# Kernel tuning notes

Hardware: AMD Instinct MI355X
Metric: run time of the kernel (lower is better)

The kernel has to match this reference:

```python
import jax, jax.numpy as jnp
import numpy as np

N_NODES = 200000
N_EDGES = 6400000
N_GRAPHS = 512
DIM_IN = 128
HID = 32
BN_EPS = 1e-5


def _gin(x, src, dst, w1, b1, w2, b2):
    # GINConv with eps=0: MLP(x + sum_{j in N(i)} x_j)
    agg = jax.ops.segment_sum(x[src], dst, num_segments=N_NODES)
    h = x + agg
    h = jnp.maximum(h @ w1 + b1, 0.0)
    return h @ w2 + b2


def _bn(x, gamma, beta):
    # BatchNorm1d, training mode: batch stats, biased variance
    m = jnp.mean(x, axis=0)
    v = jnp.var(x, axis=0)
    return gamma * (x - m) * jax.lax.rsqrt(v + BN_EPS) + beta


def setup_inputs() -> dict:
    key = jax.random.key(0)
    ks = jax.random.split(key, 20)
    s = 0.1
    inp = {
        "x": jax.random.normal(ks[0], (N_NODES, DIM_IN), jnp.float32),
        "edge_index": jax.random.randint(ks[1], (2, N_EDGES), 0, N_NODES, jnp.int32),
        "batch": jnp.sort(jax.random.randint(ks[2], (N_NODES,), 0, N_GRAPHS, jnp.int32)),
        "e0_w1": s * jax.random.normal(ks[3], (DIM_IN, HID), jnp.float32),
        "e0_b1": s * jax.random.normal(ks[4], (HID,), jnp.float32),
        "e0_w2": s * jax.random.normal(ks[5], (HID, HID), jnp.float32),
        "e0_b2": s * jax.random.normal(ks[6], (HID,), jnp.float32),
        "enc_w1": s * jax.random.normal(ks[7], (4, HID, HID), jnp.float32),
        "enc_b1": s * jax.random.normal(ks[8], (4, HID), jnp.float32),
        "enc_w2": s * jax.random.normal(ks[9], (4, HID, HID), jnp.float32),
        "enc_b2": s * jax.random.normal(ks[10], (4, HID), jnp.float32),
        "enc_gamma": jnp.ones((5, HID), jnp.float32),
        "enc_beta": jnp.zeros((5, HID), jnp.float32),
        "dec_w1": s * jax.random.normal(ks[11], (5, HID, HID), jnp.float32),
        "dec_b1": s * jax.random.normal(ks[12], (5, HID), jnp.float32),
        "dec_w2": s * jax.random.normal(ks[13], (4, HID, HID), jnp.float32),
        "dec_b2": s * jax.random.normal(ks[14], (4, HID), jnp.float32),
        "dec_w2_last": s * jax.random.normal(ks[15], (HID, DIM_IN), jnp.float32),
        "dec_b2_last": s * jax.random.normal(ks[16], (DIM_IN,), jnp.float32),
        "dec_gamma": jnp.ones((4, HID), jnp.float32),
        "dec_beta": jnp.zeros((4, HID), jnp.float32),
    }
    return inp


def reference(x, edge_index, batch,
              e0_w1, e0_b1, e0_w2, e0_b2,
              enc_w1, enc_b1, enc_w2, enc_b2, enc_gamma, enc_beta,
              dec_w1, dec_b1, dec_w2, dec_b2, dec_w2_last, dec_b2_last,
              dec_gamma, dec_beta):
    src, dst = edge_index[0], edge_index[1]

    # ----- Encoder: 5 GIN layers, ReLU then BN, collect per-layer reps -----
    xs = []
    h = jnp.maximum(_gin(x, src, dst, e0_w1, e0_b1, e0_w2, e0_b2), 0.0)
    h = _bn(h, enc_gamma[0], enc_beta[0])
    xs.append(h)
    for i in range(4):
        h = jnp.maximum(_gin(h, src, dst, enc_w1[i], enc_b1[i], enc_w2[i], enc_b2[i]), 0.0)
        h = _bn(h, enc_gamma[i + 1], enc_beta[i + 1])
        xs.append(h)
    encoded_rep = h

    # ----- Decoder: 5 GIN layers, ReLU; BN on all but last -----
    d = encoded_rep
    for i in range(5):
        w2 = dec_w2[i] if i < 4 else dec_w2_last
        b2 = dec_b2[i] if i < 4 else dec_b2_last
        d = jnp.maximum(_gin(d, src, dst, dec_w1[i], dec_b1[i], w2, b2), 0.0)
        if i < 4:
            d = _bn(d, dec_gamma[i], dec_beta[i])
    decoded_rep = d

    # ----- Global add pool of each encoder layer output, concat -----
    xpool = [jax.ops.segment_sum(xi, batch, num_segments=N_GRAPHS) for xi in xs]
    global_rep = jnp.concatenate(xpool, axis=1)  # [G, 5*32]

    return encoded_rep, decoded_rep, global_rep
```

## Files before the change

kernel.cpp:

```cpp
#include <hip/hip_runtime.h>
#include <hip/hip_bf16.h>
#include <hip/hip_fp16.h>
#include <string.h>

#define N_NODES  200000
#define N_EDGES  6400000
#define N_GRAPHS 512
#define DIM_IN   128
#define HID      32
#define BN_EPS   1e-5f

#define CHUNK    2048
#define NCHUNKS  98

typedef const float* fp;

__device__ __forceinline__ unsigned short f2h(float f) {
    __half h = __float2half(f);
    unsigned short u; __builtin_memcpy(&u, &h, 2); return u;
}
__device__ __forceinline__ float2 h2f2(unsigned int u) {
    __half2 h; __builtin_memcpy(&h, &u, 4);
    return __half22float2(h);
}


__global__ __launch_bounds__(256) void k_hist2(const int* __restrict__ dst,
                                               int* __restrict__ deg) {
    __shared__ int lh[12500];
    const int grp = blockIdx.x & 15;
    const int blk = blockIdx.x >> 4;
    const int lo = grp * 12500;
    for (int j = threadIdx.x; j < 12500; j += 256) lh[j] = 0;
    __syncthreads();
    const int4* d4 = reinterpret_cast<const int4*>(dst) + blk * 100000;
    for (int j = threadIdx.x; j < 100000; j += 256) {
        int4 v = d4[j];
        int a;
        a = v.x - lo; if ((unsigned)a < 12500u) atomicAdd(&lh[a], 1);
        a = v.y - lo; if ((unsigned)a < 12500u) atomicAdd(&lh[a], 1);
        a = v.z - lo; if ((unsigned)a < 12500u) atomicAdd(&lh[a], 1);
        a = v.w - lo; if ((unsigned)a < 12500u) atomicAdd(&lh[a], 1);
    }
    __syncthreads();
    for (int j = threadIdx.x; j < 12500; j += 256) {
        int c = lh[j];
        if (c) atomicAdd(&deg[lo + j], c);
    }
}

__global__ void k_chunksum(const int* __restrict__ deg, int* __restrict__ chunksum) {
    __shared__ int red[256];
    int b = blockIdx.x, t = threadIdx.x;
    int base = b * CHUNK;
    int s = 0;
    for (int k = 0; k < 8; ++k) {
        int i = base + t + k * 256;
        if (i < N_NODES) s += deg[i];
    }
    red[t] = s; __syncthreads();
    for (int off = 128; off > 0; off >>= 1) {
        if (t < off) red[t] += red[t + off];
        __syncthreads();
    }
    if (t == 0) chunksum[b] = red[0];
}

__global__ void k_scanchunks(const int* __restrict__ chunksum, int* __restrict__ chunkoff,
                             int* __restrict__ rowptr) {
    __shared__ int buf[128];
    int t = threadIdx.x;
    int v = (t < NCHUNKS) ? chunksum[t] : 0;
    buf[t] = v; __syncthreads();
    for (int off = 1; off < 128; off <<= 1) {
        int add = (t >= off) ? buf[t - off] : 0;
        __syncthreads();
        buf[t] += add;
        __syncthreads();
    }
    if (t < NCHUNKS) chunkoff[t] = buf[t] - v;
    if (t == 0) rowptr[N_NODES] = N_EDGES;
}

__global__ void k_scanfinal(const int* __restrict__ deg, const int* __restrict__ chunkoff,
                            int* __restrict__ rowptr, int* __restrict__ fillpos) {
    __shared__ int tsum[256];
    int b = blockIdx.x, t = threadIdx.x;
    int base = b * CHUNK + t * 8;
    int v[8]; int s = 0;
    for (int k = 0; k < 8; ++k) {
        int i = base + k;
        v[k] = (i < N_NODES) ? deg[i] : 0;
        s += v[k];
    }
    tsum[t] = s; __syncthreads();
    for (int off = 1; off < 256; off <<= 1) {
        int add = (t >= off) ? tsum[t - off] : 0;
        __syncthreads();
        tsum[t] += add;
        __syncthreads();
    }
    int run = tsum[t] - s + chunkoff[b];
    for (int k = 0; k < 8; ++k) {
        int i = base + k;
        if (i < N_NODES) { rowptr[i] = run; fillpos[i] = run; run += v[k]; }
    }
}

__global__ __launch_bounds__(256) void k_fill2(
    const int* __restrict__ src, const int* __restrict__ dst,
    int* __restrict__ fillpos, int* __restrict__ csr)
{
    const int grp = blockIdx.x & 7;
    const int blk = blockIdx.x >> 3;
    const int lo = grp * 25000, hi = lo + 25000;
    const int4* d4 = reinterpret_cast<const int4*>(dst) + blk * 12500;
    const int4* s4 = reinterpret_cast<const int4*>(src) + blk * 12500;
    for (int j = threadIdx.x; j < 12500; j += 256) {
        int4 d = d4[j];
        int4 s = s4[j];
        if (d.x >= lo && d.x < hi) { int p = atomicAdd(&fillpos[d.x], 1); csr[p] = s.x; }
        if (d.y >= lo && d.y < hi) { int p = atomicAdd(&fillpos[d.y], 1); csr[p] = s.y; }
        if (d.z >= lo && d.z < hi) { int p = atomicAdd(&fillpos[d.z], 1); csr[p] = s.z; }
        if (d.w >= lo && d.w < hi) { int p = atomicAdd(&fillpos[d.w], 1); csr[p] = s.w; }
    }
}

__global__ void k_bounds(const int* __restrict__ batch, int* __restrict__ gstart) {
    int g = blockIdx.x * blockDim.x + threadIdx.x;
    if (g > N_GRAPHS) return;
    if (g == N_GRAPHS) { gstart[g] = N_NODES; return; }
    int lo = 0, hi = N_NODES;
    while (lo < hi) {
        int mid = (lo + hi) >> 1;
        if (batch[mid] < g) lo = mid + 1; else hi = mid;
    }
    gstart[g] = lo;
}


__global__ __launch_bounds__(256) void k_proj128(
    const float* __restrict__ x, fp w1, float* __restrict__ y,
    unsigned short* __restrict__ y16)
{
    __shared__ float w1s[DIM_IN * 32];
    for (int i = threadIdx.x; i < DIM_IN * 32; i += 256) w1s[i] = w1[i];
    __syncthreads();
    const int lane = threadIdx.x & 63;
    const int c = lane & 31;
    const int srcBase = lane & 32;
    int worker   = (blockIdx.x * blockDim.x + threadIdx.x) >> 5;
    int nworkers = (gridDim.x * blockDim.x) >> 5;
    for (int n = worker; n < N_NODES; n += nworkers) {
        const float* xr = x + (size_t)n * DIM_IN;
        float x0 = xr[c], x1 = xr[32 + c], x2 = xr[64 + c], x3 = xr[96 + c];
        float acc = 0.f;
        #pragma unroll
        for (int k = 0; k < 32; ++k) {
            acc = fmaf(__shfl(x0, srcBase | k, 64), w1s[k * 32 + c], acc);
            acc = fmaf(__shfl(x1, srcBase | k, 64), w1s[(32 + k) * 32 + c], acc);
            acc = fmaf(__shfl(x2, srcBase | k, 64), w1s[(64 + k) * 32 + c], acc);
            acc = fmaf(__shfl(x3, srcBase | k, 64), w1s[(96 + k) * 32 + c], acc);
        }
        y[(size_t)n * 32 + c] = acc;
        y16[(size_t)n * 32 + c] = f2h(acc);
    }
}


__global__ __launch_bounds__(256) void k_gather16(
    const float* __restrict__ h, const unsigned short* __restrict__ h16,
    const int* __restrict__ rowptr, const int* __restrict__ csr,
    float* __restrict__ sout)
{
    const int lane = threadIdx.x & 63;
    const int sub = lane & 15;
    const int srcBase = lane & 48;
    const unsigned int* hp = reinterpret_cast<const unsigned int*>(h16);
    const float2* hs = reinterpret_cast<const float2*>(h);
    float2* so = reinterpret_cast<float2*>(sout);
    int worker   = (blockIdx.x * blockDim.x + threadIdx.x) >> 4;
    int nworkers = (gridDim.x * blockDim.x) >> 4;
    for (int n = worker; n < N_NODES; n += nworkers) {
        int e0 = rowptr[n], e1 = rowptr[n + 1];
        float2 self = hs[(size_t)n * 16 + sub];
        float a0 = self.x, a1 = self.y;
        int e = e0;
        while (e < e1) {
            int rem = e1 - e;
            int cnt = rem < 16 ? rem : 16;
            int myidx = (sub < cnt) ? csr[e + sub] : 0;
            int k = 0;
            for (; k + 8 <= cnt; k += 8) {
                int i0 = __shfl(myidx, srcBase | (k + 0), 64);
                int i1 = __shfl(myidx, srcBase | (k + 1), 64);
                int i2 = __shfl(myidx, srcBase | (k + 2), 64);
                int i3 = __shfl(myidx, srcBase | (k + 3), 64);
                int i4 = __shfl(myidx, srcBase | (k + 4), 64);
                int i5 = __shfl(myidx, srcBase | (k + 5), 64);
                int i6 = __shfl(myidx, srcBase | (k + 6), 64);
                int i7 = __shfl(myidx, srcBase | (k + 7), 64);
                unsigned int u0 = hp[(size_t)i0 * 16 + sub];
                unsigned int u1 = hp[(size_t)i1 * 16 + sub];
                unsigned int u2 = hp[(size_t)i2 * 16 + sub];
                unsigned int u3 = hp[(size_t)i3 * 16 + sub];
                unsigned int u4 = hp[(size_t)i4 * 16 + sub];
                unsigned int u5 = hp[(size_t)i5 * 16 + sub];
                unsigned int u6 = hp[(size_t)i6 * 16 + sub];
                unsigned int u7 = hp[(size_t)i7 * 16 + sub];
                float2 f0 = h2f2(u0), f1 = h2f2(u1), f2 = h2f2(u2), f3 = h2f2(u3);
                float2 f4 = h2f2(u4), f5 = h2f2(u5), f6 = h2f2(u6), f7 = h2f2(u7);
                a0 += ((f0.x + f1.x) + (f2.x + f3.x)) + ((f4.x + f5.x) + (f6.x + f7.x));
                a1 += ((f0.y + f1.y) + (f2.y + f3.y)) + ((f4.y + f5.y) + (f6.y + f7.y));
            }
            for (; k < cnt; ++k) {
                int s = __shfl(myidx, srcBase | k, 64);
                float2 f = h2f2(hp[(size_t)s * 16 + sub]);
                a0 += f.x; a1 += f.y;
            }
            e += cnt;
        }
        float2 o; o.x = a0; o.y = a1;
        so[(size_t)n * 16 + sub] = o;
    }
}


__global__ __launch_bounds__(256) void k_mlp32(
    float* __restrict__ s, fp w1, fp b1, fp w2, fp b2, float* __restrict__ stats)
{
    const int lane = threadIdx.x & 63;
    const int c = lane & 31;
    const int srcBase = lane & 32;
    float w1r[32], w2r[32];
    #pragma unroll
    for (int k = 0; k < 32; ++k) {
        w1r[k] = w1[k * 32 + c];
        w2r[k] = w2[k * 32 + c];
    }
    const float b1c = b1[c];
    const float b2c = b2[c];
    int worker   = (blockIdx.x * blockDim.x + threadIdx.x) >> 5;
    int nworkers = (gridDim.x * blockDim.x) >> 5;
    float s1 = 0.f, s2 = 0.f;
    for (int n = worker; n < N_NODES; n += nworkers) {
        float sv = s[(size_t)n * 32 + c];
        float acc1 = b1c;
        #pragma unroll
        for (int k = 0; k < 32; ++k)
            acc1 = fmaf(__shfl(sv, srcBase | k, 64), w1r[k], acc1);
        float h3 = fmaxf(acc1, 0.f);
        float acc2 = b2c;
        #pragma unroll
        for (int k = 0; k < 32; ++k)
            acc2 = fmaf(__shfl(h3, srcBase | k, 64), w2r[k], acc2);
        float a = fmaxf(acc2, 0.f);
        s[(size_t)n * 32 + c] = a;
        s1 += a; s2 += a * a;
    }
    s1 += __shfl_xor(s1, 32, 64);
    s2 += __shfl_xor(s2, 32, 64);
    __shared__ float ls1[4][32], ls2[4][32];
    int w = threadIdx.x >> 6;
    if ((threadIdx.x & 32) == 0) { ls1[w][c] = s1; ls2[w][c] = s2; }
    __syncthreads();
    if (threadIdx.x < 32) {
        float t1 = ls1[0][c] + ls1[1][c] + ls1[2][c] + ls1[3][c];
        float t2 = ls2[0][c] + ls2[1][c] + ls2[2][c] + ls2[3][c];
        atomicAdd(&stats[c], t1);
        atomicAdd(&stats[32 + c], t2);
    }
}

__global__ __launch_bounds__(256) void k_mlp0(
    float* __restrict__ s, fp b1, fp w2, fp b2, float* __restrict__ stats)
{
    const int lane = threadIdx.x & 63;
    const int c = lane & 31;
    const int srcBase = lane & 32;
    float w2r[32];
    #pragma unroll
    for (int k = 0; k < 32; ++k) w2r[k] = w2[k * 32 + c];
    const float b1c = b1[c];
    const float b2c = b2[c];
    int worker   = (blockIdx.x * blockDim.x + threadIdx.x) >> 5;
    int nworkers = (gridDim.x * blockDim.x) >> 5;
    float s1 = 0.f, s2 = 0.f;
    for (int n = worker; n < N_NODES; n += nworkers) {
        float sv = s[(size_t)n * 32 + c];
        float h3 = fmaxf(sv + b1c, 0.f);
        float acc2 = b2c;
        #pragma unroll
        for (int k = 0; k < 32; ++k)
            acc2 = fmaf(__shfl(h3, srcBase | k, 64), w2r[k], acc2);
        float a = fmaxf(acc2, 0.f);
        s[(size_t)n * 32 + c] = a;
        s1 += a; s2 += a * a;
    }
    s1 += __shfl_xor(s1, 32, 64);
    s2 += __shfl_xor(s2, 32, 64);
    __shared__ float ls1[4][32], ls2[4][32];
    int w = threadIdx.x >> 6;
    if ((threadIdx.x & 32) == 0) { ls1[w][c] = s1; ls2[w][c] = s2; }
    __syncthreads();
    if (threadIdx.x < 32) {
        float t1 = ls1[0][c] + ls1[1][c] + ls1[2][c] + ls1[3][c];
        float t2 = ls2[0][c] + ls2[1][c] + ls2[2][c] + ls2[3][c];
        atomicAdd(&stats[c], t1);
        atomicAdd(&stats[32 + c], t2);
    }
}

__global__ __launch_bounds__(256) void k_mlp_last(
    const float* __restrict__ s, fp w1, fp b1, fp w2 , fp b2,
    float* __restrict__ out)
{
    const int lane = threadIdx.x & 63;
    const int c = lane & 31;
    float w1r[32], w2a[32], w2b[32];
    #pragma unroll
    for (int k = 0; k < 32; ++k) {
        w1r[k] = w1[k * 32 + c];
        w2a[k] = w2[k * 128 + 2 * lane];
        w2b[k] = w2[k * 128 + 2 * lane + 1];
    }
    const float b1c = b1[c];
    const float b2a = b2[2 * lane];
    const float b2b = b2[2 * lane + 1];
    int worker   = (blockIdx.x * blockDim.x + threadIdx.x) >> 6;
    int nworkers = (gridDim.x * blockDim.x) >> 6;
    for (int n = worker; n < N_NODES; n += nworkers) {
        float sv = s[(size_t)n * 32 + c];
        float acc1 = b1c;
        #pragma unroll
        for (int k = 0; k < 32; ++k)
            acc1 = fmaf(__shfl(sv, k, 64), w1r[k], acc1);
        float h3 = fmaxf(acc1, 0.f);
        float oa = b2a, ob = b2b;
        #pragma unroll
        for (int k = 0; k < 32; ++k) {
            float v = __shfl(h3, (lane & 32) | k, 64);
            oa = fmaf(v, w2a[k], oa);
            ob = fmaf(v, w2b[k], ob);
        }
        oa = fmaxf(oa, 0.f); ob = fmaxf(ob, 0.f);
        float2 pr; pr.x = oa; pr.y = ob;
        reinterpret_cast<float2*>(out)[(size_t)n * 64 + lane] = pr;
    }
}

__global__ void k_bn(const float* __restrict__ a, const float* __restrict__ stats,
                     fp gamma, fp beta, float* __restrict__ hout,
                     unsigned short* __restrict__ h16out,
                     float* __restrict__ out_mirror)
{
    const int c = threadIdx.x & 31;
    float m  = stats[c] * (1.f / N_NODES);
    float vv = stats[32 + c] * (1.f / N_NODES) - m * m;
    float sc = gamma[c] / sqrtf(vv + BN_EPS);
    float sh = beta[c] - m * sc;
    int i = blockIdx.x * blockDim.x + threadIdx.x;
    int stride = gridDim.x * blockDim.x;
    for (; i < N_NODES * 32; i += stride) {
        float val = fmaf(a[i], sc, sh);
        hout[i] = val;
        h16out[i] = f2h(val);
        if (out_mirror) out_mirror[i] = val;
    }
}

__global__ void k_pool(const float* __restrict__ h, const int* __restrict__ gstart,
                       float* __restrict__ out, int col0)
{
    int g = blockIdx.x;
    int t = threadIdx.x;
    int f = t & 31, j = t >> 5;
    int n0 = gstart[g], n1 = gstart[g + 1];
    float s = 0.f;
    for (int n = n0 + j; n < n1; n += 8) s += h[(size_t)n * 32 + f];
    __shared__ float red[8][32];
    red[j][f] = s; __syncthreads();
    if (t < 32) {
        float tot = 0.f;
        #pragma unroll
        for (int k = 0; k < 8; ++k) tot += red[k][f];
        out[g * (5 * HID) + col0 + f] = tot;
    }
}


extern "C" void kernel_launch(void* const* d_in, const int* in_sizes, int n_in,
                              void* d_out, int out_size, void* d_ws, size_t ws_size,
                              hipStream_t stream) {
    fp         x        = (fp)d_in[0];
    const int* edge     = (const int*)d_in[1];
    const int* batch    = (const int*)d_in[2];
    fp e0_w1 = (fp)d_in[3],  e0_b1 = (fp)d_in[4];
    fp e0_w2 = (fp)d_in[5],  e0_b2 = (fp)d_in[6];
    fp enc_w1 = (fp)d_in[7],  enc_b1 = (fp)d_in[8];
    fp enc_w2 = (fp)d_in[9],  enc_b2 = (fp)d_in[10];
    fp enc_gamma = (fp)d_in[11], enc_beta = (fp)d_in[12];
    fp dec_w1 = (fp)d_in[13], dec_b1 = (fp)d_in[14];
    fp dec_w2 = (fp)d_in[15], dec_b2 = (fp)d_in[16];
    fp dec_w2_last = (fp)d_in[17], dec_b2_last = (fp)d_in[18];
    fp dec_gamma = (fp)d_in[19], dec_beta = (fp)d_in[20];

    const int* srcp = edge;
    const int* dstp = edge + N_EDGES;

    float* out_enc    = (float*)d_out;
    float* out_dec    = (float*)d_out + (size_t)N_NODES * 32;
    float* out_global = (float*)d_out + (size_t)N_NODES * 160;

    char* p = (char*)d_ws;
    auto alloc = [&](size_t bytes) -> void* {
        void* r = (void*)p;
        p += (bytes + 255) & ~(size_t)255;
        return r;
    };
    int*   rowptr   = (int*)alloc((N_NODES + 1) * sizeof(int));
    int*   fillpos  = (int*)alloc(N_NODES * sizeof(int));
    int*   deg      = (int*)alloc(N_NODES * sizeof(int));
    int*   chunksum = (int*)alloc(128 * sizeof(int));
    int*   chunkoff = (int*)alloc(128 * sizeof(int));
    int*   gstart   = (int*)alloc((N_GRAPHS + 1) * sizeof(int));
    float* stats    = (float*)alloc(9 * 64 * sizeof(float));
    int*   csr      = (int*)alloc((size_t)N_EDGES * sizeof(int));
    float* hbuf     = (float*)alloc((size_t)N_NODES * 32 * sizeof(float));
    float* sbuf     = (float*)alloc((size_t)N_NODES * 32 * sizeof(float));
    unsigned short* h16 = (unsigned short*)alloc((size_t)N_NODES * 32 * sizeof(unsigned short));

    hipMemsetAsync(deg, 0, N_NODES * sizeof(int), stream);
    hipMemsetAsync(stats, 0, 9 * 64 * sizeof(float), stream);

    k_hist2<<<256, 256, 0, stream>>>(dstp, deg);
    k_chunksum<<<NCHUNKS, 256, 0, stream>>>(deg, chunksum);
    k_scanchunks<<<1, 128, 0, stream>>>(chunksum, chunkoff, rowptr);
    k_scanfinal<<<NCHUNKS, 256, 0, stream>>>(deg, chunkoff, rowptr, fillpos);
    k_fill2<<<1024, 256, 0, stream>>>(srcp, dstp, fillpos, csr);
    k_bounds<<<3, 256, 0, stream>>>(batch, gstart);

    k_proj128<<<1024, 256, 0, stream>>>(x, e0_w1, hbuf, h16);
    k_gather16<<<2048, 256, 0, stream>>>(hbuf, h16, rowptr, csr, sbuf);
    k_mlp0<<<1024, 256, 0, stream>>>(sbuf, e0_b1, e0_w2, e0_b2, stats);
    k_bn<<<4096, 256, 0, stream>>>(sbuf, stats, enc_gamma, enc_beta, hbuf, h16, nullptr);
    k_pool<<<N_GRAPHS, 256, 0, stream>>>(hbuf, gstart, out_global, 0);

    for (int i = 0; i < 4; ++i) {
        float* st = stats + (1 + i) * 64;
        k_gather16<<<2048, 256, 0, stream>>>(hbuf, h16, rowptr, csr, sbuf);
        k_mlp32<<<1024, 256, 0, stream>>>(sbuf,
                                          enc_w1 + i * 1024, enc_b1 + i * 32,
                                          enc_w2 + i * 1024, enc_b2 + i * 32, st);
        k_bn<<<4096, 256, 0, stream>>>(sbuf, st,
                                       enc_gamma + (1 + i) * 32, enc_beta + (1 + i) * 32,
                                       hbuf, h16, (i == 3) ? out_enc : nullptr);
        k_pool<<<N_GRAPHS, 256, 0, stream>>>(hbuf, gstart, out_global, (1 + i) * 32);
    }

    for (int i = 0; i < 4; ++i) {
        float* st = stats + (5 + i) * 64;
        k_gather16<<<2048, 256, 0, stream>>>(hbuf, h16, rowptr, csr, sbuf);
        k_mlp32<<<1024, 256, 0, stream>>>(sbuf,
                                          dec_w1 + i * 1024, dec_b1 + i * 32,
                                          dec_w2 + i * 1024, dec_b2 + i * 32, st);
        k_bn<<<4096, 256, 0, stream>>>(sbuf, st,
                                       dec_gamma + i * 32, dec_beta + i * 32,
                                       hbuf, h16, nullptr);
    }

    k_gather16<<<2048, 256, 0, stream>>>(hbuf, h16, rowptr, csr, sbuf);
    k_mlp_last<<<1024, 256, 0, stream>>>(sbuf,
                                         dec_w1 + 4 * 1024, dec_b1 + 4 * 32,
                                         dec_w2_last, dec_b2_last, out_dec);
}
```

Before: 3.000 ms.

## Use nontemporal loads, unroll gather by 16, and vectorize batchnorm

Edge-index streams in histogram, fill and gather now use nontemporal loads and stores. The gather inner loop is restructured to issue 16 neighbor loads per full chunk, summed with independent partial accumulators, with a separate tail path. The BN kernel processes four features per thread with float4 and ushort4 accesses and is launched with half as many blocks. The aim is more memory-level parallelism and less cache pollution, at the cost of higher register pressure in the gather and a changed summation order.

```diff
diff --git a/kernel.cpp b/kernel.cpp
--- a/kernel.cpp
+++ b/kernel.cpp
@@ -14,6 +14,9 @@
 #define NCHUNKS  98
 
 typedef const float* fp;
+
+typedef int   vi4 __attribute__((ext_vector_type(4)));
+typedef float vf2 __attribute__((ext_vector_type(2)));
 
 __device__ __forceinline__ unsigned short f2h(float f) {
     __half h = __float2half(f);
@@ -33,9 +36,9 @@
     const int lo = grp * 12500;
     for (int j = threadIdx.x; j < 12500; j += 256) lh[j] = 0;
     __syncthreads();
-    const int4* d4 = reinterpret_cast<const int4*>(dst) + blk * 100000;
+    const vi4* d4 = reinterpret_cast<const vi4*>(dst) + blk * 100000;
     for (int j = threadIdx.x; j < 100000; j += 256) {
-        int4 v = d4[j];
+        vi4 v = __builtin_nontemporal_load(d4 + j);
         int a;
         a = v.x - lo; if ((unsigned)a < 12500u) atomicAdd(&lh[a], 1);
         a = v.y - lo; if ((unsigned)a < 12500u) atomicAdd(&lh[a], 1);
@@ -114,11 +117,11 @@
     const int grp = blockIdx.x & 7;
     const int blk = blockIdx.x >> 3;
     const int lo = grp * 25000, hi = lo + 25000;
-    const int4* d4 = reinterpret_cast<const int4*>(dst) + blk * 12500;
-    const int4* s4 = reinterpret_cast<const int4*>(src) + blk * 12500;
+    const vi4* d4 = reinterpret_cast<const vi4*>(dst) + blk * 12500;
+    const vi4* s4 = reinterpret_cast<const vi4*>(src) + blk * 12500;
     for (int j = threadIdx.x; j < 12500; j += 256) {
-        int4 d = d4[j];
-        int4 s = s4[j];
+        vi4 d = __builtin_nontemporal_load(d4 + j);
+        vi4 s = __builtin_nontemporal_load(s4 + j);
         if (d.x >= lo && d.x < hi) { int p = atomicAdd(&fillpos[d.x], 1); csr[p] = s.x; }
         if (d.y >= lo && d.y < hi) { int p = atomicAdd(&fillpos[d.y], 1); csr[p] = s.y; }
         if (d.z >= lo && d.z < hi) { int p = atomicAdd(&fillpos[d.z], 1); csr[p] = s.z; }
@@ -177,51 +180,49 @@
     const int sub = lane & 15;
     const int srcBase = lane & 48;
     const unsigned int* hp = reinterpret_cast<const unsigned int*>(h16);
-    const float2* hs = reinterpret_cast<const float2*>(h);
-    float2* so = reinterpret_cast<float2*>(sout);
+    const vf2* hs = reinterpret_cast<const vf2*>(h);
+    vf2* so = reinterpret_cast<vf2*>(sout);
     int worker   = (blockIdx.x * blockDim.x + threadIdx.x) >> 4;
     int nworkers = (gridDim.x * blockDim.x) >> 4;
     for (int n = worker; n < N_NODES; n += nworkers) {
         int e0 = rowptr[n], e1 = rowptr[n + 1];
-        float2 self = hs[(size_t)n * 16 + sub];
+        vf2 self = __builtin_nontemporal_load(hs + (size_t)n * 16 + sub);
         float a0 = self.x, a1 = self.y;
         int e = e0;
         while (e < e1) {
             int rem = e1 - e;
-            int cnt = rem < 16 ? rem : 16;
-            int myidx = (sub < cnt) ? csr[e + sub] : 0;
-            int k = 0;
-            for (; k + 8 <= cnt; k += 8) {
-                int i0 = __shfl(myidx, srcBase | (k + 0), 64);
-                int i1 = __shfl(myidx, srcBase | (k + 1), 64);
-                int i2 = __shfl(myidx, srcBase | (k + 2), 64);
-                int i3 = __shfl(myidx, srcBase | (k + 3), 64);
-                int i4 = __shfl(myidx, srcBase | (k + 4), 64);
-                int i5 = __shfl(myidx, srcBase | (k + 5), 64);
-                int i6 = __shfl(myidx, srcBase | (k + 6), 64);
-                int i7 = __shfl(myidx, srcBase | (k + 7), 64);
-                unsigned int u0 = hp[(size_t)i0 * 16 + sub];
-                unsigned int u1 = hp[(size_t)i1 * 16 + sub];
-                unsigned int u2 = hp[(size_t)i2 * 16 + sub];
-                unsigned int u3 = hp[(size_t)i3 * 16 + sub];
-                unsigned int u4 = hp[(size_t)i4 * 16 + sub];
-                unsigned int u5 = hp[(size_t)i5 * 16 + sub];
-                unsigned int u6 = hp[(size_t)i6 * 16 + sub];
-                unsigned int u7 = hp[(size_t)i7 * 16 + sub];
-                float2 f0 = h2f2(u0), f1 = h2f2(u1), f2 = h2f2(u2), f3 = h2f2(u3);
-                float2 f4 = h2f2(u4), f5 = h2f2(u5), f6 = h2f2(u6), f7 = h2f2(u7);
-                a0 += ((f0.x + f1.x) + (f2.x + f3.x)) + ((f4.x + f5.x) + (f6.x + f7.x));
-                a1 += ((f0.y + f1.y) + (f2.y + f3.y)) + ((f4.y + f5.y) + (f6.y + f7.y));
+            if (rem >= 16) {
+                int myidx = __builtin_nontemporal_load(csr + e + sub);
+                unsigned int u[16];
+                #pragma unroll
+                for (int k = 0; k < 16; ++k) {
+                    int s = __shfl(myidx, srcBase | k, 64);
+                    u[k] = hp[(size_t)s * 16 + sub];
+                }
+                float s0 = 0.f, s1 = 0.f, s2 = 0.f, s3 = 0.f;
+                float t0 = 0.f, t1 = 0.f, t2 = 0.f, t3 = 0.f;
+                #pragma unroll
+                for (int k = 0; k < 16; k += 4) {
+                    float2 f0 = h2f2(u[k]), f1 = h2f2(u[k + 1]);
+                    float2 f2v = h2f2(u[k + 2]), f3 = h2f2(u[k + 3]);
+                    s0 += f0.x; s1 += f1.x; s2 += f2v.x; s3 += f3.x;
+                    t0 += f0.y; t1 += f1.y; t2 += f2v.y; t3 += f3.y;
+                }
+                a0 += (s0 + s1) + (s2 + s3);
+                a1 += (t0 + t1) + (t2 + t3);
+                e += 16;
+            } else {
+                int myidx = (sub < rem) ? __builtin_nontemporal_load(csr + e + sub) : 0;
+                for (int k = 0; k < rem; ++k) {
+                    int s = __shfl(myidx, srcBase | k, 64);
+                    float2 f = h2f2(hp[(size_t)s * 16 + sub]);
+                    a0 += f.x; a1 += f.y;
+                }
+                e = e1;
             }
-            for (; k < cnt; ++k) {
-                int s = __shfl(myidx, srcBase | k, 64);
-                float2 f = h2f2(hp[(size_t)s * 16 + sub]);
-                a0 += f.x; a1 += f.y;
-            }
-            e += cnt;
         }
-        float2 o; o.x = a0; o.y = a1;
-        so[(size_t)n * 16 + sub] = o;
+        vf2 o; o.x = a0; o.y = a1;
+        __builtin_nontemporal_store(o, so + (size_t)n * 16 + sub);
     }
 }
 
@@ -354,18 +355,34 @@
                      unsigned short* __restrict__ h16out,
                      float* __restrict__ out_mirror)
 {
-    const int c = threadIdx.x & 31;
-    float m  = stats[c] * (1.f / N_NODES);
-    float vv = stats[32 + c] * (1.f / N_NODES) - m * m;
-    float sc = gamma[c] / sqrtf(vv + BN_EPS);
-    float sh = beta[c] - m * sc;
-    int i = blockIdx.x * blockDim.x + threadIdx.x;
+    int t = blockIdx.x * blockDim.x + threadIdx.x;
+    const int fb = (t & 7) * 4;
+    float sc[4], sh[4];
+    #pragma unroll
+    for (int j = 0; j < 4; ++j) {
+        int c = fb + j;
+        float m  = stats[c] * (1.f / N_NODES);
+        float vv = stats[32 + c] * (1.f / N_NODES) - m * m;
+        sc[j] = gamma[c] / sqrtf(vv + BN_EPS);
+        sh[j] = beta[c] - m * sc[j];
+    }
+    const float4* av = reinterpret_cast<const float4*>(a);
+    float4* hv = reinterpret_cast<float4*>(hout);
+    ushort4* h16v = reinterpret_cast<ushort4*>(h16out);
+    float4* mv = reinterpret_cast<float4*>(out_mirror);
     int stride = gridDim.x * blockDim.x;
-    for (; i < N_NODES * 32; i += stride) {
-        float val = fmaf(a[i], sc, sh);
-        hout[i] = val;
-        h16out[i] = f2h(val);
-        if (out_mirror) out_mirror[i] = val;
+    for (int i = t; i < N_NODES * 8; i += stride) {
+        float4 v = av[i];
+        float4 r;
+        r.x = fmaf(v.x, sc[0], sh[0]);
+        r.y = fmaf(v.y, sc[1], sh[1]);
+        r.z = fmaf(v.z, sc[2], sh[2]);
+        r.w = fmaf(v.w, sc[3], sh[3]);
+        hv[i] = r;
+        ushort4 hh;
+        hh.x = f2h(r.x); hh.y = f2h(r.y); hh.z = f2h(r.z); hh.w = f2h(r.w);
+        h16v[i] = hh;
+        if (out_mirror) mv[i] = r;
     }
 }
 
@@ -443,7 +460,7 @@
     k_proj128<<<1024, 256, 0, stream>>>(x, e0_w1, hbuf, h16);
     k_gather16<<<2048, 256, 0, stream>>>(hbuf, h16, rowptr, csr, sbuf);
     k_mlp0<<<1024, 256, 0, stream>>>(sbuf, e0_b1, e0_w2, e0_b2, stats);
-    k_bn<<<4096, 256, 0, stream>>>(sbuf, stats, enc_gamma, enc_beta, hbuf, h16, nullptr);
+    k_bn<<<2048, 256, 0, stream>>>(sbuf, stats, enc_gamma, enc_beta, hbuf, h16, nullptr);
     k_pool<<<N_GRAPHS, 256, 0, stream>>>(hbuf, gstart, out_global, 0);
 
     for (int i = 0; i < 4; ++i) {
@@ -452,7 +469,7 @@
         k_mlp32<<<1024, 256, 0, stream>>>(sbuf,
                                           enc_w1 + i * 1024, enc_b1 + i * 32,
                                           enc_w2 + i * 1024, enc_b2 + i * 32, st);
-        k_bn<<<4096, 256, 0, stream>>>(sbuf, st,
+        k_bn<<<2048, 256, 0, stream>>>(sbuf, st,
                                        enc_gamma + (1 + i) * 32, enc_beta + (1 + i) * 32,
                                        hbuf, h16, (i == 3) ? out_enc : nullptr);
         k_pool<<<N_GRAPHS, 256, 0, stream>>>(hbuf, gstart, out_global, (1 + i) * 32);
@@ -464,7 +481,7 @@
         k_mlp32<<<1024, 256, 0, stream>>>(sbuf,
                                           dec_w1 + i * 1024, dec_b1 + i * 32,
                                           dec_w2 + i * 1024, dec_b2 + i * 32, st);
-        k_bn<<<4096, 256, 0, stream>>>(sbuf, st,
+        k_bn<<<2048, 256, 0, stream>>>(sbuf, st,
                                        dec_gamma + i * 32, dec_beta + i * 32,
                                        hbuf, h16, nullptr);
     }
```

After: 3.102 ms. +3.4%, slower.
